# Optimization experiments

Hardware: AMD Instinct MI355X
Metric: run time of the kernel (lower is better)

## Reference

```python
import jax, jax.numpy as jnp
import numpy as np

N_NODES = 50000
N_EDGES = 800000
D = 128


def gcn_conv(x, edge_index, W, b, num_nodes):
    # PyG GCNConv: h = D^{-1/2} (A + I) D^{-1/2} (x @ W) + b
    xw = x @ W  # [N, D]
    src, dst = edge_index[0], edge_index[1]
    loop = jnp.arange(num_nodes, dtype=src.dtype)
    src = jnp.concatenate([src, loop])
    dst = jnp.concatenate([dst, loop])
    deg = jax.ops.segment_sum(jnp.ones_like(dst, dtype=xw.dtype), dst,
                              num_segments=num_nodes)  # [N]
    dinv = jnp.where(deg > 0, jax.lax.rsqrt(deg), 0.0)
    norm = dinv[src] * dinv[dst]  # [E+N]
    msg = xw[src] * norm[:, None]  # gather + scale, [E+N, D]
    agg = jax.ops.segment_sum(msg, dst, num_segments=num_nodes)  # scatter-add
    return agg + b


def setup_inputs() -> dict:
    key = jax.random.key(0)
    ks = jax.random.split(key, 8)
    s = 1.0 / np.sqrt(D)
    return {
        "x": jax.random.normal(ks[0], (N_NODES, D), dtype=jnp.float32),
        "edge_index": jax.random.randint(ks[1], (2, N_EDGES), 0, N_NODES, dtype=jnp.int32),
        "Wg": jax.random.normal(ks[2], (D, D), dtype=jnp.float32) * s,
        "bg": jnp.zeros((D,), dtype=jnp.float32),
        "W1": jax.random.normal(ks[3], (D, 128), dtype=jnp.float32) * s,
        "b1": jnp.zeros((128,), dtype=jnp.float32),
        "W2": jax.random.normal(ks[4], (128, 64), dtype=jnp.float32) * (1.0 / np.sqrt(128)),
        "b2": jnp.zeros((64,), dtype=jnp.float32),
        "W3": jax.random.normal(ks[5], (64, 2), dtype=jnp.float32) * (1.0 / np.sqrt(64)),
        "b3": jnp.zeros((2,), dtype=jnp.float32),
    }


def reference(x, edge_index, Wg, bg, W1, b1, W2, b2, W3, b3):
    out = jax.nn.relu(gcn_conv(x, edge_index, Wg, bg, x.shape[0]))
    h = out + x  # residual
    h = jax.nn.relu(h @ W1 + b1)
    h = jax.nn.relu(h @ W2 + b2)
    h = h @ W3 + b3  # [N, 2]
    return (h[:, 0], h[:, 1])
```

## Files before the change

kernel.cpp:

```cpp
#include <hip/hip_runtime.h>

#define TD 256
#define BCAP 3072
#define BINB 96

typedef unsigned int uint;
typedef unsigned short ushort;
typedef __attribute__((ext_vector_type(8))) short bf16x8;
typedef __attribute__((ext_vector_type(4))) float f32x4;

__device__ __forceinline__ ushort f2bf(float f) {
    uint u = __float_as_uint(f);
    u += 0x7fffu + ((u >> 16) & 1u);
    return (ushort)(u >> 16);
}
__device__ __forceinline__ float2 bfp2f(uint u) {
    float2 r;
    r.x = __uint_as_float(u << 16);
    r.y = __uint_as_float(u & 0xffff0000u);
    return r;
}

__global__ __launch_bounds__(256) void k_prep_bin(
        const float* __restrict__ Wg, const float* __restrict__ W1,
        const float* __restrict__ W2,
        ushort* __restrict__ Wgf, ushort* __restrict__ W1f, ushort* __restrict__ W2f,
        const int* __restrict__ src, const int* __restrict__ dst, int e,
        int nbuck, int* __restrict__ bucketCursor, uint* __restrict__ binned) {
    __shared__ int hist[512];
    __shared__ int base[512];
    __shared__ int cur[512];
    int t = threadIdx.x;

    if (blockIdx.x < BINB) {
        int per = (e + BINB - 1) / BINB;
        int e0 = blockIdx.x * per;
        int e1 = min(e0 + per, e);
        for (int i = t; i < nbuck; i += TD) hist[i] = 0;
        __syncthreads();
        for (int i = e0 + t; i < e1; i += TD)
            atomicAdd(&hist[dst[i] >> 7], 1);
        __syncthreads();
        for (int i = t; i < nbuck; i += TD) {
            int c = hist[i];
            base[i] = (c > 0) ? atomicAdd(&bucketCursor[i], c) : 0;
            cur[i] = 0;
        }
        __syncthreads();
        for (int i = e0 + t; i < e1; i += TD) {
            int d = dst[i];
            int b = d >> 7;
            int pos = base[b] + atomicAdd(&cur[b], 1);
            if (pos < BCAP)
                binned[(size_t)b * BCAP + pos] = ((uint)src[i] << 7) | (uint)(d & 127);
        }
    } else {
        int tid0 = (blockIdx.x - BINB) * TD + t;
        int stride = (gridDim.x - BINB) * TD;
        for (int id = tid0; id < 2048; id += stride) {
            int lane = id & 63;
            int col = ((id >> 8) << 4) + (lane & 15);
            int k0 = ((id >> 6) & 3) * 32 + (lane >> 4) * 8;
            #pragma unroll
            for (int j = 0; j < 8; j++) {
                Wgf[id * 8 + j] = f2bf(Wg[(k0 + j) * 128 + col]);
                W1f[id * 8 + j] = f2bf(W1[(k0 + j) * 128 + col]);
            }
        }
        for (int id = tid0; id < 1024; id += stride) {
            int lane = id & 63;
            int col = ((id >> 8) << 4) + (lane & 15);
            int k0 = ((id >> 6) & 3) * 32 + (lane >> 4) * 8;
            #pragma unroll
            for (int j = 0; j < 8; j++)
                W2f[id * 8 + j] = f2bf(W2[(k0 + j) * 64 + col]);
        }
    }
}

__global__ __launch_bounds__(256) void kb_fill(const int* __restrict__ bucketCursor,
                                               const uint* __restrict__ binned,
                                               int n, int nbuck,
                                               int* __restrict__ deg,
                                               int* __restrict__ rowStart,
                                               float* __restrict__ dinv,
                                               int* __restrict__ csr) {
    __shared__ int d128[128];
    __shared__ int sc[128];
    __shared__ int rs128[128];
    __shared__ int cur128[128];
    __shared__ int wsum[4];
    int b = blockIdx.x;
    int t = threadIdx.x;

    int part = 0;
    for (int i = t; i < b; i += TD) part += bucketCursor[i];
    #pragma unroll
    for (int m = 1; m < 64; m <<= 1) part += __shfl_xor(part, m);
    if ((t & 63) == 0) wsum[t >> 6] = part;
    if (t < 128) { d128[t] = 0; cur128[t] = 0; }
    __syncthreads();
    int base = wsum[0] + wsum[1] + wsum[2] + wsum[3];
    int cnt = min(bucketCursor[b], BCAP);
    int node0 = b << 7;

    for (int i = t; i < cnt; i += TD)
        atomicAdd(&d128[binned[(size_t)b * BCAP + i] & 127], 1);
    __syncthreads();
    int v = (t < 128) ? d128[t] : 0;
    if (t < 128) sc[t] = v;
    __syncthreads();
    for (int off = 1; off < 128; off <<= 1) {
        int u = (t < 128 && t >= off) ? sc[t - off] : 0;
        __syncthreads();
        if (t < 128) sc[t] += u;
        __syncthreads();
    }
    if (t < 128) {
        int node = node0 + t;
        if (node < n) {
            int rs = base + sc[t] - v;
            rs128[t] = rs;
            rowStart[node] = rs;
            deg[node] = v;
            dinv[node] = rsqrtf((float)(v + 1));
        }
    }
    __syncthreads();
    for (int i = t; i < cnt; i += TD) {
        uint pk = binned[(size_t)b * BCAP + i];
        int loc = pk & 127;
        int slot = rs128[loc] + atomicAdd(&cur128[loc], 1);
        csr[slot] = (int)(pk >> 7);
    }
}

__global__ __launch_bounds__(256) void k_xw(const float* __restrict__ x,
                                            const ushort* __restrict__ Wgf,
                                            const float* __restrict__ dinv,
                                            ushort* __restrict__ xws,
                                            int n, int nt16) {
    __shared__ __align__(16) ushort sW[16384];
    int t = threadIdx.x;
    for (int i = t; i < 2048; i += TD)
        ((float4*)sW)[i] = ((const float4*)Wgf)[i];
    __syncthreads();

    int wave = t >> 6, lane = t & 63;
    int quad = lane >> 4, m = lane & 15;

    for (int tile = blockIdx.x * 4 + wave; tile < nt16; tile += gridDim.x * 4) {
        int row0 = tile * 16;
        int arow = min(row0 + m, n - 1);
        const float* pa = x + (size_t)arow * 128 + quad * 8;
        bf16x8 af[4];
        #pragma unroll
        for (int kc = 0; kc < 4; kc++) {
            float4 f0 = *(const float4*)(pa + kc * 32);
            float4 f1 = *(const float4*)(pa + kc * 32 + 4);
            union { bf16x8 v; ushort u[8]; } tmp;
            tmp.u[0] = f2bf(f0.x); tmp.u[1] = f2bf(f0.y);
            tmp.u[2] = f2bf(f0.z); tmp.u[3] = f2bf(f0.w);
            tmp.u[4] = f2bf(f1.x); tmp.u[5] = f2bf(f1.y);
            tmp.u[6] = f2bf(f1.z); tmp.u[7] = f2bf(f1.w);
            af[kc] = tmp.v;
        }
        int orow[4]; float dv[4];
        #pragma unroll
        for (int i = 0; i < 4; i++) {
            orow[i] = row0 + quad * 4 + i;
            dv[i] = (orow[i] < n) ? dinv[orow[i]] : 0.f;
        }
        #pragma unroll
        for (int c16 = 0; c16 < 8; c16++) {
            f32x4 acc = {0.f, 0.f, 0.f, 0.f};
            #pragma unroll
            for (int kc = 0; kc < 4; kc++) {
                bf16x8 bf = *(const bf16x8*)&sW[((c16 * 4 + kc) * 64 + lane) * 8];
                acc = __builtin_amdgcn_mfma_f32_16x16x32_bf16(af[kc], bf, acc, 0, 0, 0);
            }
            int col = c16 * 16 + m;
            #pragma unroll
            for (int i = 0; i < 4; i++)
                if (orow[i] < n)
                    xws[(size_t)orow[i] * 128 + col] = f2bf(acc[i] * dv[i]);
        }
    }
}

__global__ __launch_bounds__(256) void k_agg(const uint* __restrict__ xws,
                                             const float* __restrict__ x,
                                             const int* __restrict__ rowStart,
                                             const int* __restrict__ deg,
                                             const int* __restrict__ csr,
                                             const float* __restrict__ dinv,
                                             const float* __restrict__ bg,
                                             ushort* __restrict__ h0b, int n) {
    int wave = threadIdx.x >> 6;
    int lane = threadIdx.x & 63;
    int node = blockIdx.x * 4 + wave;
    if (node >= n) return;
    float2 A0, A1 = {0.f,0.f}, A2 = {0.f,0.f}, A3 = {0.f,0.f};
    A0 = bfp2f(xws[(size_t)node * 64 + lane]);
    int st = rowStart[node];
    int cnt = deg[node];
    int i = 0;
    for (; i + 8 <= cnt; i += 8) {
        int s0 = csr[st + i + 0], s1 = csr[st + i + 1];
        int s2 = csr[st + i + 2], s3 = csr[st + i + 3];
        int s4 = csr[st + i + 4], s5 = csr[st + i + 5];
        int s6 = csr[st + i + 6], s7 = csr[st + i + 7];
        uint u0 = xws[(size_t)s0 * 64 + lane];
        uint u1 = xws[(size_t)s1 * 64 + lane];
        uint u2 = xws[(size_t)s2 * 64 + lane];
        uint u3 = xws[(size_t)s3 * 64 + lane];
        uint u4 = xws[(size_t)s4 * 64 + lane];
        uint u5 = xws[(size_t)s5 * 64 + lane];
        uint u6 = xws[(size_t)s6 * 64 + lane];
        uint u7 = xws[(size_t)s7 * 64 + lane];
        float2 v0 = bfp2f(u0), v1 = bfp2f(u1), v2 = bfp2f(u2), v3 = bfp2f(u3);
        float2 v4 = bfp2f(u4), v5 = bfp2f(u5), v6 = bfp2f(u6), v7 = bfp2f(u7);
        A0.x += v0.x; A0.y += v0.y;  A1.x += v1.x; A1.y += v1.y;
        A2.x += v2.x; A2.y += v2.y;  A3.x += v3.x; A3.y += v3.y;
        A0.x += v4.x; A0.y += v4.y;  A1.x += v5.x; A1.y += v5.y;
        A2.x += v6.x; A2.y += v6.y;  A3.x += v7.x; A3.y += v7.y;
    }
    for (; i < cnt; i++) {
        int s = csr[st + i];
        float2 v = bfp2f(xws[(size_t)s * 64 + lane]);
        A0.x += v.x; A0.y += v.y;
    }
    float2 acc;
    acc.x = (A0.x + A1.x) + (A2.x + A3.x);
    acc.y = (A0.y + A1.y) + (A2.y + A3.y);
    float dv = dinv[node];
    float2 b = ((const float2*)bg)[lane];
    float2 xv = ((const float2*)x)[(size_t)node * 64 + lane];
    float ox = fmaxf(acc.x * dv + b.x, 0.f) + xv.x;
    float oy = fmaxf(acc.y * dv + b.y, 0.f) + xv.y;
    uint up = ((uint)f2bf(oy) << 16) | (uint)f2bf(ox);
    ((uint*)h0b)[(size_t)node * 64 + lane] = up;
}

__global__ __launch_bounds__(256) void k_mlp(const ushort* __restrict__ h0b,
                                             const ushort* __restrict__ W1f,
                                             const ushort* __restrict__ W2f,
                                             const float* __restrict__ b1,
                                             const float* __restrict__ b2,
                                             const float* __restrict__ W3,
                                             const float* __restrict__ b3,
                                             float* __restrict__ out,
                                             int n, int nt16) {
    __shared__ __align__(16) ushort sW1[16384];
    __shared__ __align__(16) ushort tb[4][16 * 136];
    int t = threadIdx.x;
    for (int i = t; i < 2048; i += TD)
        ((float4*)sW1)[i] = ((const float4*)W1f)[i];
    __syncthreads();

    int wave = t >> 6, lane = t & 63;
    int quad = lane >> 4, m = lane & 15;
    ushort* tw = &tb[wave][0];

    float bc1[8];
    #pragma unroll
    for (int c = 0; c < 8; c++) bc1[c] = b1[c * 16 + m];
    float bc2[4], w30[4], w31[4];
    #pragma unroll
    for (int c = 0; c < 4; c++) {
        int col = c * 16 + m;
        bc2[c] = b2[col];
        w30[c] = W3[col * 2 + 0];
        w31[c] = W3[col * 2 + 1];
    }
    float b30 = b3[0], b31 = b3[1];

    for (int tile = blockIdx.x * 4 + wave; tile < nt16; tile += gridDim.x * 4) {
        int row0 = tile * 16;
        int arow = min(row0 + m, n - 1);
        const ushort* pa = h0b + (size_t)arow * 128 + quad * 8;
        bf16x8 af[4];
        #pragma unroll
        for (int kc = 0; kc < 4; kc++)
            af[kc] = *(const bf16x8*)(pa + kc * 32);

        #pragma unroll
        for (int c16 = 0; c16 < 8; c16++) {
            f32x4 acc = {0.f, 0.f, 0.f, 0.f};
            #pragma unroll
            for (int kc = 0; kc < 4; kc++) {
                bf16x8 bf = *(const bf16x8*)&sW1[((c16 * 4 + kc) * 64 + lane) * 8];
                acc = __builtin_amdgcn_mfma_f32_16x16x32_bf16(af[kc], bf, acc, 0, 0, 0);
            }
            int col = c16 * 16 + m;
            #pragma unroll
            for (int i = 0; i < 4; i++)
                tw[(quad * 4 + i) * 136 + col] = f2bf(fmaxf(acc[i] + bc1[c16], 0.f));
        }

        bf16x8 a2[4];
        #pragma unroll
        for (int kc = 0; kc < 4; kc++)
            a2[kc] = *(const bf16x8*)&tw[m * 136 + kc * 32 + quad * 8];

        float p0[4] = {}, p1[4] = {};
        #pragma unroll
        for (int c16 = 0; c16 < 4; c16++) {
            f32x4 acc = {0.f, 0.f, 0.f, 0.f};
            #pragma unroll
            for (int kc = 0; kc < 4; kc++) {
                bf16x8 bf = *(const bf16x8*)&W2f[((c16 * 4 + kc) * 64 + lane) * 8];
                acc = __builtin_amdgcn_mfma_f32_16x16x32_bf16(a2[kc], bf, acc, 0, 0, 0);
            }
            #pragma unroll
            for (int i = 0; i < 4; i++) {
                float h2 = fmaxf(acc[i] + bc2[c16], 0.f);
                p0[i] += h2 * w30[c16];
                p1[i] += h2 * w31[c16];
            }
        }
        #pragma unroll
        for (int i = 0; i < 4; i++) {
            #pragma unroll
            for (int msk = 1; msk < 16; msk <<= 1) {
                p0[i] += __shfl_xor(p0[i], msk);
                p1[i] += __shfl_xor(p1[i], msk);
            }
        }
        if (m == 0) {
            #pragma unroll
            for (int i = 0; i < 4; i++) {
                int r = row0 + quad * 4 + i;
                if (r < n) {
                    out[r] = p0[i] + b30;
                    out[(size_t)n + r] = p1[i] + b31;
                }
            }
        }
    }
}


extern "C" void kernel_launch(void* const* d_in, const int* in_sizes, int n_in,
                              void* d_out, int out_size, void* d_ws, size_t ws_size,
                              hipStream_t stream) {
    const float* x  = (const float*)d_in[0];
    const int*   ei = (const int*)d_in[1];
    const float* Wg = (const float*)d_in[2];
    const float* bg = (const float*)d_in[3];
    const float* W1 = (const float*)d_in[4];
    const float* b1 = (const float*)d_in[5];
    const float* W2 = (const float*)d_in[6];
    const float* b2 = (const float*)d_in[7];
    const float* W3 = (const float*)d_in[8];
    const float* b3 = (const float*)d_in[9];
    float* out = (float*)d_out;

    int n = in_sizes[0] / 128;
    int e = in_sizes[1] / 2;
    const int* src = ei;
    const int* dst = ei + e;

    char* ws = (char*)d_ws;
    size_t off = 0;
    auto alloc = [&](size_t bytes) -> void* {
        void* p = ws + off;
        off = (off + bytes + 255) & ~(size_t)255;
        return p;
    };
    int nbuck = (n + 127) >> 7;
    int*    deg      = (int*)alloc(sizeof(int) * (size_t)n);
    int*    rowStart = (int*)alloc(sizeof(int) * (size_t)n);
    float*  dinv     = (float*)alloc(sizeof(float) * (size_t)n);
    int*    bucketCursor = (int*)alloc(sizeof(int) * 512);
    uint*   binned   = (uint*)alloc(sizeof(uint) * (size_t)nbuck * BCAP);
    int*    csr      = (int*)alloc(sizeof(int) * (size_t)e);
    ushort* xws      = (ushort*)alloc(sizeof(ushort) * (size_t)n * 128);
    ushort* h0b      = (ushort*)alloc(sizeof(ushort) * (size_t)n * 128);
    ushort* Wgf      = (ushort*)alloc(sizeof(ushort) * 16384);
    ushort* W1f      = (ushort*)alloc(sizeof(ushort) * 16384);
    ushort* W2f      = (ushort*)alloc(sizeof(ushort) * 8192);
    (void)ws_size; (void)n_in; (void)out_size;

    int nt16 = (n + 15) / 16;

    hipMemsetAsync(bucketCursor, 0, sizeof(int) * 512, stream);
    hipLaunchKernelGGL(k_prep_bin, dim3(BINB + 20), dim3(TD), 0, stream,
                       Wg, W1, W2, Wgf, W1f, W2f,
                       src, dst, e, nbuck, bucketCursor, binned);
    hipLaunchKernelGGL(kb_fill, dim3(nbuck), dim3(TD), 0, stream,
                       bucketCursor, binned, n, nbuck, deg, rowStart, dinv, csr);
    hipLaunchKernelGGL(k_xw,    dim3(784), dim3(TD), 0, stream, x, Wgf, dinv, xws, n, nt16);
    hipLaunchKernelGGL(k_agg,   dim3((n + 3) / 4), dim3(TD), 0, stream,
                       (const uint*)xws, x, rowStart, deg, csr, dinv, bg, h0b, n);
    hipLaunchKernelGGL(k_mlp,   dim3(784), dim3(TD), 0, stream,
                       h0b, W1f, W2f, b1, b2, W3, b3, out, n, nt16);
}
```

Baseline: 188.9 us.

## Fuse X·W GEMM into binning kernel by moving source dinv scaling into aggregation

The X·W GEMM no longer depends on dinv, so it moves into the front kernel and runs alongside the edge-binning blocks and weight swizzle. Source-side normalisation now happens in the aggregation loop, which loads dinv[src] per edge and uses fma. This removes a kernel launch and the serial dependency of the GEMM on the CSR fill, letting GEMM and binning overlap. The cost is an extra scattered 4-byte dinv load per edge in the gather, plus per-block Wg conversion into shared memory, which also raises the front kernel's LDS use.

```diff
diff --git a/kernel.cpp b/kernel.cpp
--- a/kernel.cpp
+++ b/kernel.cpp
@@ -3,6 +3,8 @@
 #define TD 256
 #define BCAP 3072
 #define BINB 96
+#define SWZB 8
+#define XWB  640
 
 typedef unsigned int uint;
 typedef unsigned short ushort;
@@ -21,18 +23,21 @@
     return r;
 }
 
-__global__ __launch_bounds__(256) void k_prep_bin(
+__global__ __launch_bounds__(256) void k_front(
         const float* __restrict__ Wg, const float* __restrict__ W1,
         const float* __restrict__ W2,
-        ushort* __restrict__ Wgf, ushort* __restrict__ W1f, ushort* __restrict__ W2f,
+        ushort* __restrict__ W1f, ushort* __restrict__ W2f,
+        const float* __restrict__ x, ushort* __restrict__ xws,
         const int* __restrict__ src, const int* __restrict__ dst, int e,
-        int nbuck, int* __restrict__ bucketCursor, uint* __restrict__ binned) {
-    __shared__ int hist[512];
-    __shared__ int base[512];
-    __shared__ int cur[512];
+        int nbuck, int* __restrict__ bucketCursor, uint* __restrict__ binned,
+        int n, int nt16) {
+    __shared__ __align__(16) ushort sW[16384];
     int t = threadIdx.x;
 
     if (blockIdx.x < BINB) {
+        int* hist = (int*)sW;
+        int* base = hist + 512;
+        int* cur  = base + 512;
         int per = (e + BINB - 1) / BINB;
         int e0 = blockIdx.x * per;
         int e1 = min(e0 + per, e);
@@ -54,18 +59,19 @@
             if (pos < BCAP)
                 binned[(size_t)b * BCAP + pos] = ((uint)src[i] << 7) | (uint)(d & 127);
         }
-    } else {
+        return;
+    }
+
+    if (blockIdx.x < BINB + SWZB) {
         int tid0 = (blockIdx.x - BINB) * TD + t;
-        int stride = (gridDim.x - BINB) * TD;
+        int stride = SWZB * TD;
         for (int id = tid0; id < 2048; id += stride) {
             int lane = id & 63;
             int col = ((id >> 8) << 4) + (lane & 15);
             int k0 = ((id >> 6) & 3) * 32 + (lane >> 4) * 8;
             #pragma unroll
-            for (int j = 0; j < 8; j++) {
-                Wgf[id * 8 + j] = f2bf(Wg[(k0 + j) * 128 + col]);
+            for (int j = 0; j < 8; j++)
                 W1f[id * 8 + j] = f2bf(W1[(k0 + j) * 128 + col]);
-            }
         }
         for (int id = tid0; id < 1024; id += stride) {
             int lane = id & 63;
@@ -74,6 +80,58 @@
             #pragma unroll
             for (int j = 0; j < 8; j++)
                 W2f[id * 8 + j] = f2bf(W2[(k0 + j) * 64 + col]);
+        }
+        return;
+    }
+
+    for (int id = t; id < 2048; id += TD) {
+        int lane = id & 63;
+        int col = ((id >> 8) << 4) + (lane & 15);
+        int k0 = ((id >> 6) & 3) * 32 + (lane >> 4) * 8;
+        union { bf16x8 v; ushort u[8]; } tmp;
+        #pragma unroll
+        for (int j = 0; j < 8; j++)
+            tmp.u[j] = f2bf(Wg[(k0 + j) * 128 + col]);
+        *(bf16x8*)&sW[id * 8] = tmp.v;
+    }
+    __syncthreads();
+
+    int xwid = blockIdx.x - (BINB + SWZB);
+    int nxw = gridDim.x - (BINB + SWZB);
+    int wave = t >> 6, lane = t & 63;
+    int quad = lane >> 4, m = lane & 15;
+
+    for (int tile = xwid * 4 + wave; tile < nt16; tile += nxw * 4) {
+        int row0 = tile * 16;
+        int arow = min(row0 + m, n - 1);
+        const float* pa = x + (size_t)arow * 128 + quad * 8;
+        bf16x8 af[4];
+        #pragma unroll
+        for (int kc = 0; kc < 4; kc++) {
+            float4 f0 = *(const float4*)(pa + kc * 32);
+            float4 f1 = *(const float4*)(pa + kc * 32 + 4);
+            union { bf16x8 v; ushort u[8]; } tmp;
+            tmp.u[0] = f2bf(f0.x); tmp.u[1] = f2bf(f0.y);
+            tmp.u[2] = f2bf(f0.z); tmp.u[3] = f2bf(f0.w);
+            tmp.u[4] = f2bf(f1.x); tmp.u[5] = f2bf(f1.y);
+            tmp.u[6] = f2bf(f1.z); tmp.u[7] = f2bf(f1.w);
+            af[kc] = tmp.v;
+        }
+        #pragma unroll
+        for (int c16 = 0; c16 < 8; c16++) {
+            f32x4 acc = {0.f, 0.f, 0.f, 0.f};
+            #pragma unroll
+            for (int kc = 0; kc < 4; kc++) {
+                bf16x8 bf = *(const bf16x8*)&sW[((c16 * 4 + kc) * 64 + lane) * 8];
+                acc = __builtin_amdgcn_mfma_f32_16x16x32_bf16(af[kc], bf, acc, 0, 0, 0);
+            }
+            int col = c16 * 16 + m;
+            #pragma unroll
+            for (int i = 0; i < 4; i++) {
+                int r = row0 + quad * 4 + i;
+                if (r < n)
+                    xws[(size_t)r * 128 + col] = f2bf(acc[i]);
+            }
         }
     }
 }
@@ -135,59 +193,6 @@
     }
 }
 
-__global__ __launch_bounds__(256) void k_xw(const float* __restrict__ x,
-                                            const ushort* __restrict__ Wgf,
-                                            const float* __restrict__ dinv,
-                                            ushort* __restrict__ xws,
-                                            int n, int nt16) {
-    __shared__ __align__(16) ushort sW[16384];
-    int t = threadIdx.x;
-    for (int i = t; i < 2048; i += TD)
-        ((float4*)sW)[i] = ((const float4*)Wgf)[i];
-    __syncthreads();
-
-    int wave = t >> 6, lane = t & 63;
-    int quad = lane >> 4, m = lane & 15;
-
-    for (int tile = blockIdx.x * 4 + wave; tile < nt16; tile += gridDim.x * 4) {
-        int row0 = tile * 16;
-        int arow = min(row0 + m, n - 1);
-        const float* pa = x + (size_t)arow * 128 + quad * 8;
-        bf16x8 af[4];
-        #pragma unroll
-        for (int kc = 0; kc < 4; kc++) {
-            float4 f0 = *(const float4*)(pa + kc * 32);
-            float4 f1 = *(const float4*)(pa + kc * 32 + 4);
-            union { bf16x8 v; ushort u[8]; } tmp;
-            tmp.u[0] = f2bf(f0.x); tmp.u[1] = f2bf(f0.y);
-            tmp.u[2] = f2bf(f0.z); tmp.u[3] = f2bf(f0.w);
-            tmp.u[4] = f2bf(f1.x); tmp.u[5] = f2bf(f1.y);
-            tmp.u[6] = f2bf(f1.z); tmp.u[7] = f2bf(f1.w);
-            af[kc] = tmp.v;
-        }
-        int orow[4]; float dv[4];
-        #pragma unroll
-        for (int i = 0; i < 4; i++) {
-            orow[i] = row0 + quad * 4 + i;
-            dv[i] = (orow[i] < n) ? dinv[orow[i]] : 0.f;
-        }
-        #pragma unroll
-        for (int c16 = 0; c16 < 8; c16++) {
-            f32x4 acc = {0.f, 0.f, 0.f, 0.f};
-            #pragma unroll
-            for (int kc = 0; kc < 4; kc++) {
-                bf16x8 bf = *(const bf16x8*)&sW[((c16 * 4 + kc) * 64 + lane) * 8];
-                acc = __builtin_amdgcn_mfma_f32_16x16x32_bf16(af[kc], bf, acc, 0, 0, 0);
-            }
-            int col = c16 * 16 + m;
-            #pragma unroll
-            for (int i = 0; i < 4; i++)
-                if (orow[i] < n)
-                    xws[(size_t)orow[i] * 128 + col] = f2bf(acc[i] * dv[i]);
-        }
-    }
-}
-
 __global__ __launch_bounds__(256) void k_agg(const uint* __restrict__ xws,
                                              const float* __restrict__ x,
                                              const int* __restrict__ rowStart,
@@ -200,8 +205,12 @@
     int lane = threadIdx.x & 63;
     int node = blockIdx.x * 4 + wave;
     if (node >= n) return;
+    float dv = dinv[node];
     float2 A0, A1 = {0.f,0.f}, A2 = {0.f,0.f}, A3 = {0.f,0.f};
-    A0 = bfp2f(xws[(size_t)node * 64 + lane]);
+    {
+        float2 s = bfp2f(xws[(size_t)node * 64 + lane]);
+        A0.x = dv * s.x; A0.y = dv * s.y;
+    }
     int st = rowStart[node];
     int cnt = deg[node];
     int i = 0;
@@ -210,6 +219,8 @@
         int s2 = csr[st + i + 2], s3 = csr[st + i + 3];
         int s4 = csr[st + i + 4], s5 = csr[st + i + 5];
         int s6 = csr[st + i + 6], s7 = csr[st + i + 7];
+        float d0 = dinv[s0], d1 = dinv[s1], d2 = dinv[s2], d3 = dinv[s3];
+        float d4 = dinv[s4], d5 = dinv[s5], d6 = dinv[s6], d7 = dinv[s7];
         uint u0 = xws[(size_t)s0 * 64 + lane];
         uint u1 = xws[(size_t)s1 * 64 + lane];
         uint u2 = xws[(size_t)s2 * 64 + lane];
@@ -220,20 +231,24 @@
         uint u7 = xws[(size_t)s7 * 64 + lane];
         float2 v0 = bfp2f(u0), v1 = bfp2f(u1), v2 = bfp2f(u2), v3 = bfp2f(u3);
         float2 v4 = bfp2f(u4), v5 = bfp2f(u5), v6 = bfp2f(u6), v7 = bfp2f(u7);
-        A0.x += v0.x; A0.y += v0.y;  A1.x += v1.x; A1.y += v1.y;
-        A2.x += v2.x; A2.y += v2.y;  A3.x += v3.x; A3.y += v3.y;
-        A0.x += v4.x; A0.y += v4.y;  A1.x += v5.x; A1.y += v5.y;
-        A2.x += v6.x; A2.y += v6.y;  A3.x += v7.x; A3.y += v7.y;
+        A0.x = fmaf(d0, v0.x, A0.x); A0.y = fmaf(d0, v0.y, A0.y);
+        A1.x = fmaf(d1, v1.x, A1.x); A1.y = fmaf(d1, v1.y, A1.y);
+        A2.x = fmaf(d2, v2.x, A2.x); A2.y = fmaf(d2, v2.y, A2.y);
+        A3.x = fmaf(d3, v3.x, A3.x); A3.y = fmaf(d3, v3.y, A3.y);
+        A0.x = fmaf(d4, v4.x, A0.x); A0.y = fmaf(d4, v4.y, A0.y);
+        A1.x = fmaf(d5, v5.x, A1.x); A1.y = fmaf(d5, v5.y, A1.y);
+        A2.x = fmaf(d6, v6.x, A2.x); A2.y = fmaf(d6, v6.y, A2.y);
+        A3.x = fmaf(d7, v7.x, A3.x); A3.y = fmaf(d7, v7.y, A3.y);
     }
     for (; i < cnt; i++) {
         int s = csr[st + i];
+        float ds = dinv[s];
         float2 v = bfp2f(xws[(size_t)s * 64 + lane]);
-        A0.x += v.x; A0.y += v.y;
+        A0.x = fmaf(ds, v.x, A0.x); A0.y = fmaf(ds, v.y, A0.y);
     }
     float2 acc;
     acc.x = (A0.x + A1.x) + (A2.x + A3.x);
     acc.y = (A0.y + A1.y) + (A2.y + A3.y);
-    float dv = dinv[node];
     float2 b = ((const float2*)bg)[lane];
     float2 xv = ((const float2*)x)[(size_t)node * 64 + lane];
     float ox = fmaxf(acc.x * dv + b.x, 0.f) + xv.x;
@@ -377,7 +392,6 @@
     int*    csr      = (int*)alloc(sizeof(int) * (size_t)e);
     ushort* xws      = (ushort*)alloc(sizeof(ushort) * (size_t)n * 128);
     ushort* h0b      = (ushort*)alloc(sizeof(ushort) * (size_t)n * 128);
-    ushort* Wgf      = (ushort*)alloc(sizeof(ushort) * 16384);
     ushort* W1f      = (ushort*)alloc(sizeof(ushort) * 16384);
     ushort* W2f      = (ushort*)alloc(sizeof(ushort) * 8192);
     (void)ws_size; (void)n_in; (void)out_size;
@@ -385,12 +399,11 @@
     int nt16 = (n + 15) / 16;
 
     hipMemsetAsync(bucketCursor, 0, sizeof(int) * 512, stream);
-    hipLaunchKernelGGL(k_prep_bin, dim3(BINB + 20), dim3(TD), 0, stream,
-                       Wg, W1, W2, Wgf, W1f, W2f,
-                       src, dst, e, nbuck, bucketCursor, binned);
+    hipLaunchKernelGGL(k_front, dim3(BINB + SWZB + XWB), dim3(TD), 0, stream,
+                       Wg, W1, W2, W1f, W2f, x, xws,
+                       src, dst, e, nbuck, bucketCursor, binned, n, nt16);
     hipLaunchKernelGGL(kb_fill, dim3(nbuck), dim3(TD), 0, stream,
                        bucketCursor, binned, n, nbuck, deg, rowStart, dinv, csr);
-    hipLaunchKernelGGL(k_xw,    dim3(784), dim3(TD), 0, stream, x, Wgf, dinv, xws, n, nt16);
     hipLaunchKernelGGL(k_agg,   dim3((n + 3) / 4), dim3(TD), 0, stream,
                        (const uint*)xws, x, rowStart, deg, csr, dinv, bg, h0b, n);
     hipLaunchKernelGGL(k_mlp,   dim3(784), dim3(TD), 0, stream,
```

Result: faster. 180.1 us (-4.7%).
